# Kernel optimization log

Hardware: AMD Instinct MI355X
Metric: run time of the kernel (lower is better)

## Reference

```python
import jax, jax.numpy as jnp
import numpy as np

B, N, IN_DIM, HID = 32, 1024, 128, 64


def setup_inputs() -> dict:
    key = jax.random.key(0)
    ks = jax.random.split(key, 12)
    s_in = 1.0 / np.sqrt(IN_DIM)
    s_h = 1.0 / np.sqrt(HID)
    return {
        "x": jax.random.normal(ks[0], (B, N, IN_DIM), dtype=jnp.float32),
        "A": jax.random.uniform(ks[1], (B, N, N), dtype=jnp.float32),
        # fc_hidden: input_dim -> hidden_dim
        "W_h": jax.random.uniform(ks[2], (IN_DIM, HID), jnp.float32, -s_in, s_in),
        "b_h": jax.random.uniform(ks[3], (HID,), jnp.float32, -s_in, s_in),
        # fc_1 inside Gated_Skip_Connection (input_dim != output_dim)
        "W_fc1": jax.random.uniform(ks[4], (IN_DIM, HID), jnp.float32, -s_in, s_in),
        "b_fc1": jax.random.uniform(ks[5], (HID,), jnp.float32, -s_in, s_in),
        # gated_X1, gated_X2: hidden -> hidden
        "W_g1": jax.random.uniform(ks[6], (HID, HID), jnp.float32, -s_h, s_h),
        "b_g1": jax.random.uniform(ks[7], (HID,), jnp.float32, -s_h, s_h),
        "W_g2": jax.random.uniform(ks[8], (HID, HID), jnp.float32, -s_h, s_h),
        "b_g2": jax.random.uniform(ks[9], (HID,), jnp.float32, -s_h, s_h),
    }


def reference(x, A, W_h, b_h, W_fc1, b_fc1, W_g1, b_g1, W_g2, b_g2):
    # x_new = bmm(A, fc_hidden(x))   [B, N, HID]
    x_new = jnp.einsum("bnm,bmh->bnh", A, x @ W_h + b_h)
    # gated skip connection (input_dim != output_dim -> project x first)
    x_proj = x @ W_fc1 + b_fc1
    gate = jax.nn.sigmoid((x_proj @ W_g1 + b_g1) + (x_new @ W_g2 + b_g2))
    out = x_new * gate + x_proj * (1.0 - gate)
    return out
```

## Files before the change

### kernel.cpp

```cpp
#include <hip/hip_runtime.h>
#include <hip/hip_bf16.h>

#define NB 32
#define NN 1024
#define IND 128
#define HD 64

typedef float f32x4 __attribute__((ext_vector_type(4)));
typedef short bf16x8 __attribute__((ext_vector_type(8)));
typedef unsigned short ushortx4 __attribute__((ext_vector_type(4)));

union FragU { unsigned short us[8]; bf16x8 v; };

__device__ __forceinline__ unsigned short f2bf(float f) {
    union { float f; unsigned u; } x; x.f = f;
    unsigned r = x.u + 0x7FFFu + ((x.u >> 16) & 1u);
    return (unsigned short)(r >> 16);
}
__device__ __forceinline__ float bf2f(unsigned short h) {
    union { unsigned u; float f; } x; x.u = ((unsigned)h) << 16; return x.f;
}

__global__ void prep_k(const float* __restrict__ W_h, const float* __restrict__ W_fc1,
                       const float* __restrict__ W_g1, const float* __restrict__ W_g2,
                       const float* __restrict__ b_g1, const float* __restrict__ b_g2,
                       unsigned short* __restrict__ WcT_hi, unsigned short* __restrict__ WcT_lo,
                       unsigned short* __restrict__ Wg1T_hi, unsigned short* __restrict__ Wg1T_lo,
                       unsigned short* __restrict__ Wg2T_hi, unsigned short* __restrict__ Wg2T_lo,
                       float* __restrict__ biasP1) {
    int t = blockIdx.x * blockDim.x + threadIdx.x;
    if (t < 16384) {
        int o = t >> 7, k = t & 127;
        float v = (o < 64) ? W_h[k * 64 + o] : W_fc1[k * 64 + (o - 64)];
        unsigned short hi = f2bf(v);
        WcT_hi[t] = hi; WcT_lo[t] = f2bf(v - bf2f(hi));
    } else if (t < 20480) {
        int r = t - 16384; int o = r >> 6, k = r & 63;
        float v = W_g1[k * 64 + o];
        unsigned short hi = f2bf(v);
        Wg1T_hi[r] = hi; Wg1T_lo[r] = f2bf(v - bf2f(hi));
    } else if (t < 24576) {
        int r = t - 20480; int o = r >> 6, k = r & 63;
        float v = W_g2[k * 64 + o];
        unsigned short hi = f2bf(v);
        Wg2T_hi[r] = hi; Wg2T_lo[r] = f2bf(v - bf2f(hi));
    } else if (t < 24640) {
        int j = t - 24576;
        biasP1[j] = b_g1[j] + b_g2[j];
    }
}

__global__ __launch_bounds__(64) void k1(
        const float* __restrict__ x,
        const unsigned short* __restrict__ WcT_hi, const unsigned short* __restrict__ WcT_lo,
        const unsigned short* __restrict__ Wg1T_hi, const unsigned short* __restrict__ Wg1T_lo,
        const float* __restrict__ b_h, const float* __restrict__ b_fc1,
        const float* __restrict__ biasP1,
        unsigned short* __restrict__ hF, float* __restrict__ xproj,
        float* __restrict__ p1) {
    __shared__ unsigned short lds_hi[16 * 64];
    __shared__ unsigned short lds_lo[16 * 64];

    const int lane = threadIdx.x;
    const int lr = lane & 15, lg = lane >> 4;
    const int blk = blockIdx.x;
    const int b = blk >> 6;
    const int n0 = (blk & 63) * 16;

    const float* xp = x + (size_t)(b * NN + n0 + lr) * IND;

    f32x4 xa[4][2];
#pragma unroll
    for (int ks = 0; ks < 4; ks++) {
        const f32x4* ap = (const f32x4*)(xp + 32 * ks + 8 * lg);
        xa[ks][0] = ap[0]; xa[ks][1] = ap[1];
    }

    f32x4 acc[8];
#pragma unroll
    for (int f = 0; f < 8; f++) acc[f] = (f32x4){0.f, 0.f, 0.f, 0.f};

#pragma unroll
    for (int ks = 0; ks < 4; ks++) {
        FragU ah, al;
#pragma unroll
        for (int i = 0; i < 4; i++) {
            unsigned short h0 = f2bf(xa[ks][0][i]); ah.us[i] = h0;     al.us[i]     = f2bf(xa[ks][0][i] - bf2f(h0));
            unsigned short h1 = f2bf(xa[ks][1][i]); ah.us[4 + i] = h1; al.us[4 + i] = f2bf(xa[ks][1][i] - bf2f(h1));
        }
#pragma unroll
        for (int f = 0; f < 8; f++) {
            int off = (16 * f + lr) * 128 + 32 * ks + 8 * lg;
            bf16x8 wh = *(const bf16x8*)(WcT_hi + off);
            bf16x8 wl = *(const bf16x8*)(WcT_lo + off);
            acc[f] = __builtin_amdgcn_mfma_f32_16x16x32_bf16(ah.v, wh, acc[f], 0, 0, 0);
            acc[f] = __builtin_amdgcn_mfma_f32_16x16x32_bf16(ah.v, wl, acc[f], 0, 0, 0);
            acc[f] = __builtin_amdgcn_mfma_f32_16x16x32_bf16(al.v, wh, acc[f], 0, 0, 0);
        }
    }

    const int mb = n0 + 4 * lg;
    const int tile = mb >> 5;
    const int lanepart = lr + 16 * ((mb >> 3) & 3);
    const int j0 = mb & 7;

#pragma unroll
    for (int f = 0; f < 4; f++) {
        int c = 16 * f + lr;
        float bh = b_h[c];
        ushortx4 hv;
#pragma unroll
        for (int r = 0; r < 4; r++) hv[r] = f2bf(acc[f][r] + bh);
        *(ushortx4*)(hF + (size_t)b * 65536 + (size_t)(tile * 4 + f) * 512 + lanepart * 8 + j0) = hv;
    }

#pragma unroll
    for (int f = 4; f < 8; f++) {
        int c = 16 * (f - 4) + lr;
        float bp = b_fc1[c];
#pragma unroll
        for (int r = 0; r < 4; r++) {
            float v = acc[f][r] + bp;
            int n = mb + r;
            xproj[(size_t)(b * NN + n) * 64 + c] = v;
            int ln = 4 * lg + r;
            int idx = ln * 64 + (((c >> 3) ^ (ln & 7)) << 3) + (c & 7);
            unsigned short hi = f2bf(v);
            lds_hi[idx] = hi;
            lds_lo[idx] = f2bf(v - bf2f(hi));
        }
    }
    __syncthreads();

    f32x4 accP[4];
#pragma unroll
    for (int f = 0; f < 4; f++) accP[f] = (f32x4){0.f, 0.f, 0.f, 0.f};
#pragma unroll
    for (int ks = 0; ks < 2; ks++) {
        int c0 = 32 * ks + 8 * lg;
        int idx = lr * 64 + (((c0 >> 3) ^ (lr & 7)) << 3);
        bf16x8 a_hi = *(const bf16x8*)(lds_hi + idx);
        bf16x8 a_lo = *(const bf16x8*)(lds_lo + idx);
#pragma unroll
        for (int f = 0; f < 4; f++) {
            int off = (16 * f + lr) * 64 + c0;
            bf16x8 b_hi = *(const bf16x8*)(Wg1T_hi + off);
            bf16x8 b_lo = *(const bf16x8*)(Wg1T_lo + off);
            accP[f] = __builtin_amdgcn_mfma_f32_16x16x32_bf16(a_hi, b_hi, accP[f], 0, 0, 0);
            accP[f] = __builtin_amdgcn_mfma_f32_16x16x32_bf16(a_hi, b_lo, accP[f], 0, 0, 0);
            accP[f] = __builtin_amdgcn_mfma_f32_16x16x32_bf16(a_lo, b_hi, accP[f], 0, 0, 0);
        }
    }
#pragma unroll
    for (int f = 0; f < 4; f++) {
        int c = 16 * f + lr;
        float bb = biasP1[c];
#pragma unroll
        for (int r = 0; r < 4; r++) {
            int n = mb + r;
            p1[(size_t)(b * NN + n) * 64 + c] = accP[f][r] + bb;
        }
    }
}

__global__ __launch_bounds__(64) void k2(
        const float* __restrict__ A, const unsigned short* __restrict__ hF,
        const unsigned short* __restrict__ Wg2T_hi, const unsigned short* __restrict__ Wg2T_lo,
        const float* __restrict__ p1, const float* __restrict__ xproj,
        float* __restrict__ out) {
    __shared__ unsigned short tile_hi[16 * 64];
    __shared__ unsigned short tile_lo[16 * 64];

    const int lane = threadIdx.x;
    const int lr = lane & 15, lg = lane >> 4;
    const int blk = blockIdx.x;
    const int b = blk >> 6;
    const int n0 = (blk & 63) * 16;

    const float* Ap = A + (size_t)(b * NN + n0 + lr) * NN + 8 * lg;
    const unsigned short* hp = hF + (size_t)b * 65536 + lane * 8;

    f32x4 acc[4];
#pragma unroll
    for (int f = 0; f < 4; f++) acc[f] = (f32x4){0.f, 0.f, 0.f, 0.f};

    f32x4 ab[4][2];
#pragma unroll
    for (int i = 0; i < 4; i++) {
        ab[i][0] = *(const f32x4*)(Ap + 32 * i);
        ab[i][1] = *(const f32x4*)(Ap + 32 * i + 4);
    }
    bf16x8 hb[2][4];
#pragma unroll
    for (int f = 0; f < 4; f++) hb[0][f] = *(const bf16x8*)(hp + f * 512);

#pragma unroll
    for (int it = 0; it < 32; ++it) {
        FragU au;
        f32x4 c0 = ab[it & 3][0], c1 = ab[it & 3][1];
#pragma unroll
        for (int i = 0; i < 4; i++) { au.us[i] = f2bf(c0[i]); au.us[4 + i] = f2bf(c1[i]); }
#pragma unroll
        for (int f = 0; f < 4; f++)
            acc[f] = __builtin_amdgcn_mfma_f32_16x16x32_bf16(au.v, hb[it & 1][f], acc[f], 0, 0, 0);
        if (it < 31) {
#pragma unroll
            for (int f = 0; f < 4; f++)
                hb[(it + 1) & 1][f] = *(const bf16x8*)(hp + (size_t)((it + 1) * 4 + f) * 512);
        }
        if (it < 28) {
            ab[it & 3][0] = *(const f32x4*)(Ap + (it + 4) * 32);
            ab[it & 3][1] = *(const f32x4*)(Ap + (it + 4) * 32 + 4);
        }
    }

#pragma unroll
    for (int f = 0; f < 4; f++) {
        int c = 16 * f + lr;
#pragma unroll
        for (int r = 0; r < 4; r++) {
            int row = 4 * lg + r;
            int idx = row * 64 + (((c >> 3) ^ (row & 7)) << 3) + (c & 7);
            float v = acc[f][r];
            unsigned short hi = f2bf(v);
            tile_hi[idx] = hi;
            tile_lo[idx] = f2bf(v - bf2f(hi));
        }
    }
    __syncthreads();

    f32x4 accG[4];
#pragma unroll
    for (int f = 0; f < 4; f++) accG[f] = (f32x4){0.f, 0.f, 0.f, 0.f};
#pragma unroll
    for (int ks = 0; ks < 2; ks++) {
        int c0k = 32 * ks + 8 * lg;
        int idx = lr * 64 + (((c0k >> 3) ^ (lr & 7)) << 3);
        bf16x8 a_hi = *(const bf16x8*)(tile_hi + idx);
        bf16x8 a_lo = *(const bf16x8*)(tile_lo + idx);
#pragma unroll
        for (int f = 0; f < 4; f++) {
            int off = (16 * f + lr) * 64 + c0k;
            bf16x8 b_hi = *(const bf16x8*)(Wg2T_hi + off);
            bf16x8 b_lo = *(const bf16x8*)(Wg2T_lo + off);
            accG[f] = __builtin_amdgcn_mfma_f32_16x16x32_bf16(a_hi, b_hi, accG[f], 0, 0, 0);
            accG[f] = __builtin_amdgcn_mfma_f32_16x16x32_bf16(a_hi, b_lo, accG[f], 0, 0, 0);
            accG[f] = __builtin_amdgcn_mfma_f32_16x16x32_bf16(a_lo, b_hi, accG[f], 0, 0, 0);
        }
    }

#pragma unroll
    for (int f = 0; f < 4; f++) {
        int c = 16 * f + lr;
#pragma unroll
        for (int r = 0; r < 4; r++) {
            int n = n0 + 4 * lg + r;
            size_t g = (size_t)(b * NN + n) * 64 + c;
            float z = p1[g] + accG[f][r];
            float gate = 1.f / (1.f + __expf(-z));
            float xpv = xproj[g];
            out[g] = acc[f][r] * gate + xpv * (1.f - gate);
        }
    }
}

extern "C" void kernel_launch(void* const* d_in, const int* in_sizes, int n_in,
                              void* d_out, int out_size, void* d_ws, size_t ws_size,
                              hipStream_t stream) {
    const float* x     = (const float*)d_in[0];
    const float* A     = (const float*)d_in[1];
    const float* W_h   = (const float*)d_in[2];
    const float* b_h   = (const float*)d_in[3];
    const float* W_fc1 = (const float*)d_in[4];
    const float* b_fc1 = (const float*)d_in[5];
    const float* W_g1  = (const float*)d_in[6];
    const float* b_g1  = (const float*)d_in[7];
    const float* W_g2  = (const float*)d_in[8];
    const float* b_g2  = (const float*)d_in[9];
    float* out = (float*)d_out;

    char* ws = (char*)d_ws;
    unsigned short* WcT_hi  = (unsigned short*)(ws);
    unsigned short* WcT_lo  = (unsigned short*)(ws + 32768);
    unsigned short* Wg1T_hi = (unsigned short*)(ws + 65536);
    unsigned short* Wg1T_lo = (unsigned short*)(ws + 73728);
    unsigned short* Wg2T_hi = (unsigned short*)(ws + 81920);
    unsigned short* Wg2T_lo = (unsigned short*)(ws + 90112);
    float*          bP1     = (float*)(ws + 98304);
    unsigned short* hF      = (unsigned short*)(ws + 131072);
    float*          xprj    = (float*)(ws + 131072 + 4194304);
    float*          p1      = (float*)(ws + 131072 + 4194304 + 8388608);

    prep_k<<<97, 256, 0, stream>>>(W_h, W_fc1, W_g1, W_g2, b_g1, b_g2,
                                   WcT_hi, WcT_lo, Wg1T_hi, Wg1T_lo, Wg2T_hi, Wg2T_lo, bP1);
    k1<<<2048, 64, 0, stream>>>(x, WcT_hi, WcT_lo, Wg1T_hi, Wg1T_lo, b_h, b_fc1, bP1,
                                hF, xprj, p1);
    k2<<<2048, 64, 0, stream>>>(A, hF, Wg2T_hi, Wg2T_lo, p1, xprj, out);
}
```

Baseline: 65.52 us.

## Stage A and hF tiles through LDS with async triple-buffered global_load_lds

k2 now uses 256-thread blocks, each covering 64 rows, and streams A and hF chunks into shared memory with direct global-to-LDS loads in a three-slot ring. Barriers and explicit vmcnt waits gate reuse of each slot. The four waves of a block now share each hF chunk instead of every 64-thread block reloading it, and the loads run ahead asynchronously rather than through register prefetch. In exchange the kernel needs 72KB of LDS per block, which limits occupancy, and adds per-iteration block barriers.

```diff
diff --git a/kernel.cpp b/kernel.cpp
--- a/kernel.cpp
+++ b/kernel.cpp
@@ -20,6 +20,14 @@
 __device__ __forceinline__ float bf2f(unsigned short h) {
     union { unsigned u; float f; } x; x.u = ((unsigned)h) << 16; return x.f;
 }
+
+__device__ __forceinline__ void gl16(void* lds, const void* g) {
+    __builtin_amdgcn_global_load_lds(
+        (const __attribute__((address_space(1))) unsigned int*)g,
+        (__attribute__((address_space(3))) unsigned int*)lds, 16, 0, 0);
+}
+
+#define WAITVM(N) asm volatile("s_waitcnt vmcnt(" #N ")" ::: "memory")
 
 __global__ void prep_k(const float* __restrict__ W_h, const float* __restrict__ W_fc1,
                        const float* __restrict__ W_g1, const float* __restrict__ W_g2,
@@ -163,57 +171,83 @@
     }
 }
 
-__global__ __launch_bounds__(64) void k2(
+__global__ __launch_bounds__(256, 2) void k2(
         const float* __restrict__ A, const unsigned short* __restrict__ hF,
         const unsigned short* __restrict__ Wg2T_hi, const unsigned short* __restrict__ Wg2T_lo,
         const float* __restrict__ p1, const float* __restrict__ xproj,
         float* __restrict__ out) {
-    __shared__ unsigned short tile_hi[16 * 64];
-    __shared__ unsigned short tile_lo[16 * 64];
-
-    const int lane = threadIdx.x;
+    __shared__ char smem[73728];
+
+    const int tid = threadIdx.x;
+    const int w = tid >> 6, lane = tid & 63;
     const int lr = lane & 15, lg = lane >> 4;
-    const int blk = blockIdx.x;
-    const int b = blk >> 6;
-    const int n0 = (blk & 63) * 16;
-
-    const float* Ap = A + (size_t)(b * NN + n0 + lr) * NN + 8 * lg;
-    const unsigned short* hp = hF + (size_t)b * 65536 + lane * 8;
+    const int b = blockIdx.x >> 4;
+    const int rt = blockIdx.x & 15;
+
+    const float* aS[4];
+#pragma unroll
+    for (int i = 0; i < 4; i++) {
+        int rowl = w * 16 + i * 4 + lg;
+        int g = (lane & 15) ^ ((i * 4 + lg) & 15);
+        aS[i] = A + (size_t)(b * NN + rt * 64 + rowl) * NN + g * 4;
+    }
+    const unsigned short* hS[2];
+#pragma unroll
+    for (int j = 0; j < 2; j++)
+        hS[j] = hF + (size_t)b * 65536 + (w * 2 + j) * 512 + lane * 8;
+
+#define STAGE(T, SLOT)                                                        \
+    {                                                                         \
+        _Pragma("unroll")                                                     \
+        for (int i = 0; i < 4; i++)                                           \
+            gl16(smem + (SLOT) * 16384 + (w * 4 + i) * 1024, aS[i] + (T) * 64); \
+        _Pragma("unroll")                                                     \
+        for (int j = 0; j < 2; j++)                                           \
+            gl16(smem + 49152 + (SLOT) * 8192 + (w * 2 + j) * 1024, hS[j] + (T) * 4096); \
+    }
 
     f32x4 acc[4];
 #pragma unroll
     for (int f = 0; f < 4; f++) acc[f] = (f32x4){0.f, 0.f, 0.f, 0.f};
 
-    f32x4 ab[4][2];
-#pragma unroll
-    for (int i = 0; i < 4; i++) {
-        ab[i][0] = *(const f32x4*)(Ap + 32 * i);
-        ab[i][1] = *(const f32x4*)(Ap + 32 * i + 4);
-    }
-    bf16x8 hb[2][4];
-#pragma unroll
-    for (int f = 0; f < 4; f++) hb[0][f] = *(const bf16x8*)(hp + f * 512);
-
-#pragma unroll
-    for (int it = 0; it < 32; ++it) {
-        FragU au;
-        f32x4 c0 = ab[it & 3][0], c1 = ab[it & 3][1];
-#pragma unroll
-        for (int i = 0; i < 4; i++) { au.us[i] = f2bf(c0[i]); au.us[4 + i] = f2bf(c1[i]); }
-#pragma unroll
-        for (int f = 0; f < 4; f++)
-            acc[f] = __builtin_amdgcn_mfma_f32_16x16x32_bf16(au.v, hb[it & 1][f], acc[f], 0, 0, 0);
-        if (it < 31) {
-#pragma unroll
-            for (int f = 0; f < 4; f++)
-                hb[(it + 1) & 1][f] = *(const bf16x8*)(hp + (size_t)((it + 1) * 4 + f) * 512);
-        }
-        if (it < 28) {
-            ab[it & 3][0] = *(const f32x4*)(Ap + (it + 4) * 32);
-            ab[it & 3][1] = *(const f32x4*)(Ap + (it + 4) * 32 + 4);
-        }
-    }
-
+    STAGE(0, 0) STAGE(1, 1) STAGE(2, 2)
+
+    const char* Arow = smem + (w * 16 + lr) * 256;
+
+#pragma unroll
+    for (int t = 0; t < 16; ++t) {
+        const int slot = t % 3;
+        if (t < 14)      { WAITVM(12); }
+        else if (t == 14){ WAITVM(6);  }
+        else             { WAITVM(0);  }
+        __builtin_amdgcn_s_barrier();
+        __builtin_amdgcn_sched_barrier(0);
+
+#pragma unroll
+        for (int kc = 0; kc < 2; kc++) {
+            int g0 = kc * 8 + 2 * lg;
+            f32x4 a0 = *(const f32x4*)(Arow + slot * 16384 + ((g0 ^ lr) << 4));
+            f32x4 a1 = *(const f32x4*)(Arow + slot * 16384 + (((g0 + 1) ^ lr) << 4));
+            FragU au;
+#pragma unroll
+            for (int i = 0; i < 4; i++) { au.us[i] = f2bf(a0[i]); au.us[4 + i] = f2bf(a1[i]); }
+            const char* Hb = smem + 49152 + slot * 8192 + kc * 4096 + lane * 16;
+#pragma unroll
+            for (int f = 0; f < 4; f++) {
+                bf16x8 hfv = *(const bf16x8*)(Hb + f * 1024);
+                acc[f] = __builtin_amdgcn_mfma_f32_16x16x32_bf16(au.v, hfv, acc[f], 0, 0, 0);
+            }
+        }
+
+        asm volatile("s_waitcnt lgkmcnt(0)" ::: "memory");
+        __builtin_amdgcn_sched_barrier(0);
+        __builtin_amdgcn_s_barrier();
+        if (t + 3 < 16) STAGE(t + 3, slot)
+    }
+#undef STAGE
+
+    unsigned short* th = (unsigned short*)(smem + w * 4096);
+    unsigned short* tl = th + 1024;
 #pragma unroll
     for (int f = 0; f < 4; f++) {
         int c = 16 * f + lr;
@@ -223,11 +257,11 @@
             int idx = row * 64 + (((c >> 3) ^ (row & 7)) << 3) + (c & 7);
             float v = acc[f][r];
             unsigned short hi = f2bf(v);
-            tile_hi[idx] = hi;
-            tile_lo[idx] = f2bf(v - bf2f(hi));
-        }
-    }
-    __syncthreads();
+            th[idx] = hi;
+            tl[idx] = f2bf(v - bf2f(hi));
+        }
+    }
+    asm volatile("s_waitcnt lgkmcnt(0)" ::: "memory");
 
     f32x4 accG[4];
 #pragma unroll
@@ -236,8 +270,8 @@
     for (int ks = 0; ks < 2; ks++) {
         int c0k = 32 * ks + 8 * lg;
         int idx = lr * 64 + (((c0k >> 3) ^ (lr & 7)) << 3);
-        bf16x8 a_hi = *(const bf16x8*)(tile_hi + idx);
-        bf16x8 a_lo = *(const bf16x8*)(tile_lo + idx);
+        bf16x8 a_hi = *(const bf16x8*)(th + idx);
+        bf16x8 a_lo = *(const bf16x8*)(tl + idx);
 #pragma unroll
         for (int f = 0; f < 4; f++) {
             int off = (16 * f + lr) * 64 + c0k;
@@ -249,12 +283,13 @@
         }
     }
 
+    const int n0w = rt * 64 + w * 16;
 #pragma unroll
     for (int f = 0; f < 4; f++) {
         int c = 16 * f + lr;
 #pragma unroll
         for (int r = 0; r < 4; r++) {
-            int n = n0 + 4 * lg + r;
+            int n = n0w + 4 * lg + r;
             size_t g = (size_t)(b * NN + n) * 64 + c;
             float z = p1[g] + accG[f][r];
             float gate = 1.f / (1.f + __expf(-z));
@@ -295,5 +330,5 @@
                                    WcT_hi, WcT_lo, Wg1T_hi, Wg1T_lo, Wg2T_hi, Wg2T_lo, bP1);
     k1<<<2048, 64, 0, stream>>>(x, WcT_hi, WcT_lo, Wg1T_hi, Wg1T_lo, b_h, b_fc1, bP1,
                                 hF, xprj, p1);
-    k2<<<2048, 64, 0, stream>>>(A, hF, Wg2T_hi, Wg2T_lo, p1, xprj, out);
-}
+    k2<<<512, 256, 0, stream>>>(A, hF, Wg2T_hi, Wg2T_lo, p1, xprj, out);
+}
```

Result: no change. 66.24 us (+1.1%).

## Restructure A-aggregation kernel with LDS-staged async loads and 4-wave blocks

Applied to the files above, without the earlier changes.

The bmm kernel moves from one-wave blocks covering 16 rows to 256-thread blocks covering 32 rows. Each wave loads A rows directly into double-buffered LDS with global_load_lds, using an XOR swizzle, and splits the 64 output columns across waves. Block ids are remapped so each XCD works on contiguous batches, which should improve L2 reuse of the per-batch hidden features. The change is meant to raise memory-level parallelism on the large A stream, at the cost of more LDS use, extra barriers and lower occupancy per CU.

```diff
diff --git a/kernel.cpp b/kernel.cpp
--- a/kernel.cpp
+++ b/kernel.cpp
@@ -19,6 +19,12 @@
 }
 __device__ __forceinline__ float bf2f(unsigned short h) {
     union { unsigned u; float f; } x; x.u = ((unsigned)h) << 16; return x.f;
+}
+
+__device__ __forceinline__ void gl16(void* lds, const void* g) {
+    __builtin_amdgcn_global_load_lds(
+        (const __attribute__((address_space(1))) unsigned int*)g,
+        (__attribute__((address_space(3))) unsigned int*)lds, 16, 0, 0);
 }
 
 __global__ void prep_k(const float* __restrict__ W_h, const float* __restrict__ W_fc1,
@@ -163,103 +169,144 @@
     }
 }
 
-__global__ __launch_bounds__(64) void k2(
+__global__ __launch_bounds__(256, 2) void k2(
         const float* __restrict__ A, const unsigned short* __restrict__ hF,
         const unsigned short* __restrict__ Wg2T_hi, const unsigned short* __restrict__ Wg2T_lo,
         const float* __restrict__ p1, const float* __restrict__ xproj,
         float* __restrict__ out) {
-    __shared__ unsigned short tile_hi[16 * 64];
-    __shared__ unsigned short tile_lo[16 * 64];
-
-    const int lane = threadIdx.x;
+    __shared__ char smem[65536];
+
+    const int tid = threadIdx.x;
+    const int w = tid >> 6, lane = tid & 63;
     const int lr = lane & 15, lg = lane >> 4;
-    const int blk = blockIdx.x;
-    const int b = blk >> 6;
-    const int n0 = (blk & 63) * 16;
-
-    const float* Ap = A + (size_t)(b * NN + n0 + lr) * NN + 8 * lg;
-    const unsigned short* hp = hF + (size_t)b * 65536 + lane * 8;
-
-    f32x4 acc[4];
-#pragma unroll
-    for (int f = 0; f < 4; f++) acc[f] = (f32x4){0.f, 0.f, 0.f, 0.f};
-
-    f32x4 ab[4][2];
-#pragma unroll
-    for (int i = 0; i < 4; i++) {
-        ab[i][0] = *(const f32x4*)(Ap + 32 * i);
-        ab[i][1] = *(const f32x4*)(Ap + 32 * i + 4);
-    }
-    bf16x8 hb[2][4];
-#pragma unroll
-    for (int f = 0; f < 4; f++) hb[0][f] = *(const bf16x8*)(hp + f * 512);
-
-#pragma unroll
-    for (int it = 0; it < 32; ++it) {
-        FragU au;
-        f32x4 c0 = ab[it & 3][0], c1 = ab[it & 3][1];
-#pragma unroll
-        for (int i = 0; i < 4; i++) { au.us[i] = f2bf(c0[i]); au.us[4 + i] = f2bf(c1[i]); }
-#pragma unroll
-        for (int f = 0; f < 4; f++)
-            acc[f] = __builtin_amdgcn_mfma_f32_16x16x32_bf16(au.v, hb[it & 1][f], acc[f], 0, 0, 0);
-        if (it < 31) {
-#pragma unroll
-            for (int f = 0; f < 4; f++)
-                hb[(it + 1) & 1][f] = *(const bf16x8*)(hp + (size_t)((it + 1) * 4 + f) * 512);
-        }
-        if (it < 28) {
-            ab[it & 3][0] = *(const f32x4*)(Ap + (it + 4) * 32);
-            ab[it & 3][1] = *(const f32x4*)(Ap + (it + 4) * 32 + 4);
-        }
-    }
-
-#pragma unroll
-    for (int f = 0; f < 4; f++) {
-        int c = 16 * f + lr;
+    const int wr = w >> 1, wc = w & 1;
+
+    const int wgid = ((int)blockIdx.x & 7) * 128 + ((int)blockIdx.x >> 3);
+    const int b = wgid >> 5;
+    const int rt = wgid & 31;
+
+    const float* aS[8];
+#pragma unroll
+    for (int i = 0; i < 8; i++) {
+        int rl = w * 8 + i;
+        aS[i] = A + (size_t)(b * NN + rt * 32 + rl) * NN + ((lane ^ rl) << 2);
+    }
+    const unsigned short* hBase = hF + (size_t)b * 65536;
+
+    f32x4 acc[2];
+    acc[0] = (f32x4){0.f, 0.f, 0.f, 0.f};
+    acc[1] = (f32x4){0.f, 0.f, 0.f, 0.f};
+
+    bf16x8 hb[8][2];
+
+#pragma unroll
+    for (int i = 0; i < 8; i++)
+        gl16(smem + (w * 8 + i) * 1024, aS[i]);
+#pragma unroll
+    for (int ks = 0; ks < 8; ks++)
+#pragma unroll
+        for (int i = 0; i < 2; i++)
+            hb[ks][i] = *(const bf16x8*)(hBase + (size_t)(ks * 4 + 2 * wc + i) * 512 + lane * 8);
+    __syncthreads();
+
+    const int rl_c = 16 * wr + lr;
+
+#define COMPUTE(ks, Abase)                                                     \
+    {                                                                          \
+        int g0 = (ks) * 8 + lg * 2;                                            \
+        f32x4 a0 = *(const f32x4*)((Abase) + ((g0 ^ rl_c) << 4));              \
+        f32x4 a1 = *(const f32x4*)((Abase) + (((g0 + 1) ^ rl_c) << 4));        \
+        FragU au;                                                              \
+        _Pragma("unroll")                                                      \
+        for (int ii = 0; ii < 4; ii++) {                                       \
+            au.us[ii] = f2bf(a0[ii]); au.us[4 + ii] = f2bf(a1[ii]);            \
+        }                                                                      \
+        acc[0] = __builtin_amdgcn_mfma_f32_16x16x32_bf16(au.v, hb[ks][0], acc[0], 0, 0, 0); \
+        acc[1] = __builtin_amdgcn_mfma_f32_16x16x32_bf16(au.v, hb[ks][1], acc[1], 0, 0, 0); \
+    }
+
+#pragma unroll
+    for (int t = 0; t < 4; t++) {
+        const int slot = t & 1;
+        const char* Abase = smem + slot * 32768 + rl_c * 1024;
+
+        if (t < 3) {
+#pragma unroll
+            for (int i = 0; i < 8; i++)
+                gl16(smem + (slot ^ 1) * 32768 + (w * 8 + i) * 1024,
+                     aS[i] + (t + 1) * 256);
+        }
+
+        COMPUTE(0, Abase) COMPUTE(1, Abase) COMPUTE(2, Abase) COMPUTE(3, Abase)
+        if (t < 3) {
+#pragma unroll
+            for (int ks = 0; ks < 4; ks++)
+#pragma unroll
+                for (int i = 0; i < 2; i++)
+                    hb[ks][i] = *(const bf16x8*)(hBase +
+                        (size_t)(((t + 1) * 8 + ks) * 4 + 2 * wc + i) * 512 + lane * 8);
+        }
+        COMPUTE(4, Abase) COMPUTE(5, Abase) COMPUTE(6, Abase) COMPUTE(7, Abase)
+        if (t < 3) {
+#pragma unroll
+            for (int ks = 4; ks < 8; ks++)
+#pragma unroll
+                for (int i = 0; i < 2; i++)
+                    hb[ks][i] = *(const bf16x8*)(hBase +
+                        (size_t)(((t + 1) * 8 + ks) * 4 + 2 * wc + i) * 512 + lane * 8);
+        }
+        __syncthreads();
+    }
+#undef COMPUTE
+
+    unsigned short* th = (unsigned short*)(smem + wr * 4096);
+    unsigned short* tl = th + 1024;
+#pragma unroll
+    for (int i = 0; i < 2; i++) {
+        int c = 32 * wc + 16 * i + lr;
 #pragma unroll
         for (int r = 0; r < 4; r++) {
-            int row = 4 * lg + r;
-            int idx = row * 64 + (((c >> 3) ^ (row & 7)) << 3) + (c & 7);
-            float v = acc[f][r];
+            int ln = 4 * lg + r;
+            int idx = ln * 64 + (((c >> 3) ^ (ln & 7)) << 3) + (c & 7);
+            float v = acc[i][r];
             unsigned short hi = f2bf(v);
-            tile_hi[idx] = hi;
-            tile_lo[idx] = f2bf(v - bf2f(hi));
+            th[idx] = hi;
+            tl[idx] = f2bf(v - bf2f(hi));
         }
     }
     __syncthreads();
 
-    f32x4 accG[4];
-#pragma unroll
-    for (int f = 0; f < 4; f++) accG[f] = (f32x4){0.f, 0.f, 0.f, 0.f};
-#pragma unroll
-    for (int ks = 0; ks < 2; ks++) {
-        int c0k = 32 * ks + 8 * lg;
+    f32x4 accG[2];
+    accG[0] = (f32x4){0.f, 0.f, 0.f, 0.f};
+    accG[1] = (f32x4){0.f, 0.f, 0.f, 0.f};
+#pragma unroll
+    for (int ksk = 0; ksk < 2; ksk++) {
+        int c0k = 32 * ksk + 8 * lg;
         int idx = lr * 64 + (((c0k >> 3) ^ (lr & 7)) << 3);
-        bf16x8 a_hi = *(const bf16x8*)(tile_hi + idx);
-        bf16x8 a_lo = *(const bf16x8*)(tile_lo + idx);
-#pragma unroll
-        for (int f = 0; f < 4; f++) {
-            int off = (16 * f + lr) * 64 + c0k;
+        bf16x8 a_hi = *(const bf16x8*)(th + idx);
+        bf16x8 a_lo = *(const bf16x8*)(tl + idx);
+#pragma unroll
+        for (int i = 0; i < 2; i++) {
+            int off = (16 * (2 * wc + i) + lr) * 64 + c0k;
             bf16x8 b_hi = *(const bf16x8*)(Wg2T_hi + off);
             bf16x8 b_lo = *(const bf16x8*)(Wg2T_lo + off);
-            accG[f] = __builtin_amdgcn_mfma_f32_16x16x32_bf16(a_hi, b_hi, accG[f], 0, 0, 0);
-            accG[f] = __builtin_amdgcn_mfma_f32_16x16x32_bf16(a_hi, b_lo, accG[f], 0, 0, 0);
-            accG[f] = __builtin_amdgcn_mfma_f32_16x16x32_bf16(a_lo, b_hi, accG[f], 0, 0, 0);
-        }
-    }
-
-#pragma unroll
-    for (int f = 0; f < 4; f++) {
-        int c = 16 * f + lr;
+            accG[i] = __builtin_amdgcn_mfma_f32_16x16x32_bf16(a_hi, b_hi, accG[i], 0, 0, 0);
+            accG[i] = __builtin_amdgcn_mfma_f32_16x16x32_bf16(a_hi, b_lo, accG[i], 0, 0, 0);
+            accG[i] = __builtin_amdgcn_mfma_f32_16x16x32_bf16(a_lo, b_hi, accG[i], 0, 0, 0);
+        }
+    }
+
+#pragma unroll
+    for (int i = 0; i < 2; i++) {
+        int c = 16 * (2 * wc + i) + lr;
 #pragma unroll
         for (int r = 0; r < 4; r++) {
-            int n = n0 + 4 * lg + r;
+            int n = rt * 32 + 16 * wr + 4 * lg + r;
             size_t g = (size_t)(b * NN + n) * 64 + c;
-            float z = p1[g] + accG[f][r];
+            float z = p1[g] + accG[i][r];
             float gate = 1.f / (1.f + __expf(-z));
             float xpv = xproj[g];
-            out[g] = acc[f][r] * gate + xpv * (1.f - gate);
+            out[g] = acc[i][r] * gate + xpv * (1.f - gate);
         }
     }
 }
@@ -295,5 +342,5 @@
                                    WcT_hi, WcT_lo, Wg1T_hi, Wg1T_lo, Wg2T_hi, Wg2T_lo, bP1);
     k1<<<2048, 64, 0, stream>>>(x, WcT_hi, WcT_lo, Wg1T_hi, Wg1T_lo, b_h, b_fc1, bP1,
                                 hF, xprj, p1);
-    k2<<<2048, 64, 0, stream>>>(A, hF, Wg2T_hi, Wg2T_lo, p1, xprj, out);
-}
+    k2<<<1024, 256, 0, stream>>>(A, hF, Wg2T_hi, Wg2T_lo, p1, xprj, out);
+}
```

New measurement: 64.26 us. Within noise of the previous version (-1.9%).
